# Performance work log

Measured on AMD Instinct MI355X. Metric: run time of the kernel, lower is better.

Reference implementation:

```python
import jax, jax.numpy as jnp
from jax import lax
import numpy as np

A = 9                 # 3 scales x 3 ratios
PRE_NMS_TOPN = 4000
POST_NMS_TOPN = 2000
NMS_THRESH = 0.7
MIN_SIZE = 16.0       # min_size * im_scale (im_info scale = 1)
NEG_INF = -1e9


def generate_anchors(base_size=16, ratios=(0.5, 1.0, 2.0), scales=(8, 16, 32)):
    ratios = np.array(ratios, dtype=np.float64)
    scales = np.array(scales, dtype=np.float64)
    w = h = float(base_size)
    xc = yc = 0.5 * (base_size - 1)
    size = w * h
    ws_r = np.round(np.sqrt(size / ratios))          # [3]
    hs_r = np.round(ws_r * ratios)                   # [3]
    ws = (ws_r[:, None] * scales[None, :]).reshape(-1)   # [9]
    hs = (hs_r[:, None] * scales[None, :]).reshape(-1)   # [9]
    anchors = np.stack([xc - 0.5 * (ws - 1), yc - 0.5 * (hs - 1),
                        xc + 0.5 * (ws - 1), yc + 0.5 * (hs - 1)], axis=1)
    return anchors.astype(np.float32)                # [9,4]


def _conv(x, w, b, padding):
    y = lax.conv_general_dilated(x, w, (1, 1), padding,
                                 dimension_numbers=('NCHW', 'OIHW', 'NCHW'))
    return y + b[None, :, None, None]


def _bbox_transform_inv(anchors, deltas):
    w = anchors[:, 2] - anchors[:, 0] + 1.0
    h = anchors[:, 3] - anchors[:, 1] + 1.0
    cx = anchors[:, 0] + 0.5 * w
    cy = anchors[:, 1] + 0.5 * h
    pcx = deltas[:, 0] * w + cx
    pcy = deltas[:, 1] * h + cy
    pw = jnp.exp(deltas[:, 2]) * w
    ph = jnp.exp(deltas[:, 3]) * h
    return jnp.stack([pcx - 0.5 * pw, pcy - 0.5 * ph,
                      pcx + 0.5 * pw, pcy + 0.5 * ph], axis=1)


def _greedy_nms(boxes, keep_init, thresh):
    # boxes already sorted by descending score; keep_init masks invalid rows
    x1, y1, x2, y2 = boxes[:, 0], boxes[:, 1], boxes[:, 2], boxes[:, 3]
    areas = (x2 - x1 + 1.0) * (y2 - y1 + 1.0)
    xx1 = jnp.maximum(x1[:, None], x1[None, :])
    yy1 = jnp.maximum(y1[:, None], y1[None, :])
    xx2 = jnp.minimum(x2[:, None], x2[None, :])
    yy2 = jnp.minimum(y2[:, None], y2[None, :])
    inter = jnp.maximum(0.0, xx2 - xx1 + 1.0) * jnp.maximum(0.0, yy2 - yy1 + 1.0)
    iou = inter / (areas[:, None] + areas[None, :] - inter)   # [N,N]
    n = boxes.shape[0]
    idx = jnp.arange(n)

    def body(i, keep):
        suppress = keep[i] & (iou[i] > thresh) & (idx > i)
        return keep & ~suppress

    return lax.fori_loop(0, n, body, keep_init)


def reference(im, feats, w_conv, b_conv, w_cls, b_cls, w_reg, b_reg):
    im_h, im_w = im.shape[2], im.shape[3]
    fh, fw = feats.shape[2], feats.shape[3]
    stride = round(im_w / fw)

    # RPN head (classifier)
    hid = jax.nn.relu(_conv(feats, w_conv, b_conv, 'SAME'))
    rpn_map = _conv(hid, w_cls, b_cls, 'SAME')       # [1, 2A, fh, fw]
    rpn_bbox = _conv(hid, w_reg, b_reg, 'SAME')      # [1, 4A, fh, fw]

    # anchor generation: [K*A, 4], shift-major / anchor-minor
    base = jnp.asarray(generate_anchors())
    sx = jnp.arange(fw, dtype=jnp.float32) * stride
    sy = jnp.arange(fh, dtype=jnp.float32) * stride
    sxx, syy = jnp.meshgrid(sx, sy)                  # [fh, fw]
    shifts = jnp.stack([sxx.ravel(), syy.ravel(), sxx.ravel(), syy.ravel()], 1)
    anchors = (base[None, :, :] + shifts[:, None, :]).reshape(-1, 4)

    # predictions, flattened in (h, w, a) order to match anchors
    deltas = rpn_bbox.transpose(0, 2, 3, 1).reshape(-1, 4)
    scores = rpn_map[:, A:, :, :].transpose(0, 2, 3, 1).reshape(-1)

    proposals = _bbox_transform_inv(anchors, deltas)
    # clip_boxes to image
    proposals = jnp.stack([
        jnp.clip(proposals[:, 0], 0.0, im_w - 1.0),
        jnp.clip(proposals[:, 1], 0.0, im_h - 1.0),
        jnp.clip(proposals[:, 2], 0.0, im_w - 1.0),
        jnp.clip(proposals[:, 3], 0.0, im_h - 1.0)], axis=1)

    # filter_boxes (min_size) expressed as a score mask (jit-friendly)
    ws = proposals[:, 2] - proposals[:, 0] + 1.0
    hs = proposals[:, 3] - proposals[:, 1] + 1.0
    valid = (ws >= MIN_SIZE) & (hs >= MIN_SIZE)
    masked_scores = jnp.where(valid, scores, NEG_INF)

    # sort descending, take pre_nms_topN
    order = jnp.argsort(-masked_scores)[:PRE_NMS_TOPN]
    top_boxes = proposals[order]
    top_scores = masked_scores[order]
    keep_init = top_scores > NEG_INF / 2

    keep = _greedy_nms(top_boxes, keep_init, NMS_THRESH)

    # take first post_nms_topN kept (already in score order), padded with zeros
    rank = jnp.cumsum(keep) - 1
    take = keep & (rank < POST_NMS_TOPN)
    dst = jnp.where(take, rank, 0)
    out_boxes = jnp.zeros((POST_NMS_TOPN, 4), dtype=top_boxes.dtype)
    out_boxes = out_boxes.at[dst].add(jnp.where(take[:, None], top_boxes, 0.0))
    out_scores = jnp.zeros((POST_NMS_TOPN, 1), dtype=top_scores.dtype)
    out_scores = out_scores.at[dst].add(jnp.where(take[:, None], top_scores[:, None], 0.0))
    return out_boxes, out_scores


def setup_inputs() -> dict:
    key = jax.random.key(0)
    ks = jax.random.split(key, 8)
    # small weight scale keeps exp(dw) in a sane range, as a trained RPN would
    return {
        'im': jax.random.normal(ks[0], (1, 3, 800, 1216), jnp.float32),
        'feats': jax.random.normal(ks[1], (1, 1024, 50, 76), jnp.float32),
        'w_conv': jax.random.normal(ks[2], (512, 1024, 3, 3), jnp.float32) * 0.001,
        'b_conv': jnp.zeros((512,), jnp.float32),
        'w_cls': jax.random.normal(ks[3], (18, 512, 1, 1), jnp.float32) * 0.01,
        'b_cls': jnp.zeros((18,), jnp.float32),
        'w_reg': jax.random.normal(ks[4], (36, 512, 1, 1), jnp.float32) * 0.01,
        'b_reg': jnp.zeros((36,), jnp.float32),
    }
```

## Files before the change

kernel.cpp:

```cpp
#include <hip/hip_runtime.h>
#include <stdint.h>
#include <math.h>

typedef unsigned long long u64;
typedef unsigned int u32;

#define CIN     1024
#define COUT    512
#define FH      50
#define FW      76
#define QP      80
#define HIDP    4096
#define FPITCH  4160
#define NPOS    3800
#define NA      34200
#define PRE_N   4000
#define POST_N  2000
#define MASKW   63
#define TBN     4032
#define KSLICES 8
#define CPS     128
#define QT      128
#define SPP     (CPS/2)

#define P0 (3*CIN*FPITCH)
#define P2 (512*48)
#define P3 65536
#define PREP_BLKS ((P0+P2+P3)/256)
#define WT_BLKS   (144*8)

__device__ __forceinline__ void async16(const float* g, float* l) {
  __builtin_amdgcn_global_load_lds(
      (__attribute__((address_space(1))) void*)(g),
      (__attribute__((address_space(3))) void*)(l), 16, 0, 0);
}

__global__ void k_prep(const float* __restrict__ feats, const float* __restrict__ w_conv,
                       const float* __restrict__ w_cls, const float* __restrict__ b_cls,
                       const float* __restrict__ w_reg, const float* __restrict__ b_reg,
                       float* __restrict__ fpad3, float* __restrict__ wt,
                       float* __restrict__ wT, float* __restrict__ bT,
                       u32* __restrict__ hist, u32* __restrict__ ctrl,
                       double4* __restrict__ tb, float* __restrict__ ts) {
  __shared__ float t[64][65];
  if (blockIdx.x >= PREP_BLKS) {
    int bt_ = blockIdx.x - PREP_BLKS;
    int kx = bt_ % 144, oy = bt_ / 144;
    int k0 = kx * 64, oc0 = oy * 64;
    int tx = threadIdx.x & 63, tg = threadIdx.x >> 6;
#pragma unroll
    for (int rr = 0; rr < 16; rr++) {
      int row = tg * 16 + rr;
      t[row][tx] = w_conv[(size_t)(oc0 + row) * 9216 + k0 + tx];
    }
    __syncthreads();
#pragma unroll
    for (int rr = 0; rr < 16; rr++) {
      int kr = tg * 16 + rr;
      wt[(size_t)(k0 + kr) * 512 + oc0 + tx] = t[tx][kr];
    }
    return;
  }
  int idx = blockIdx.x * 256 + threadIdx.x;
  if (idx < P0) {
    int tc = idx / (CIN * FPITCH);
    int rem = idx - tc * (CIN * FPITCH);
    int cin = rem / FPITCH;
    int j = rem - cin * FPITCH + tc;
    float v = 0.f;
    if (j < FPITCH) {
      int r = j / QP, u = j - r * QP;
      if (r >= 1 && r <= FH && u >= 1 && u <= FW)
        v = feats[cin * (FH * FW) + (r - 1) * FW + (u - 1)];
    }
    fpad3[idx] = v;
    return;
  }
  idx -= P0;
  if (idx < P2) {
    int c = idx / 48, o = idx - c * 48;
    float v = 0.f;
    if (o < 9) v = w_cls[(size_t)(9 + o) * 512 + c];
    else if (o < 45) v = w_reg[(size_t)(o - 9) * 512 + c];
    wT[idx] = v;
    return;
  }
  idx -= P2;
  if (idx < P3) {
    hist[idx] = 0;
    if (idx < 8) ctrl[idx] = 0;
    if (idx < 48) bT[idx] = (idx < 9) ? b_cls[9 + idx] : (idx < 45 ? b_reg[idx - 9] : 0.f);
    if (idx >= PRE_N && idx < TBN) { tb[idx] = make_double4(0.0, 0.0, 0.0, 0.0); ts[idx] = -1.0e9f; }
  }
}

__global__ __launch_bounds__(256, 6) void k_conv(const float* __restrict__ fpad3,
                                                 const float* __restrict__ wt,
                                                 float* __restrict__ hidp) {
  __shared__ __align__(16) float Bl[2][2][10][QT];
  const int tid = threadIdx.x;
  const int lane = tid & 63;
  const int wv = __builtin_amdgcn_readfirstlane(tid >> 6);
  const int q0 = blockIdx.x * QT;
  const int ws = (blockIdx.y << 2) + wv;
  const int c0 = blockIdx.z * CPS;

  int rA = 2 * wv + (lane >> 5);
  int trA = rA / 3, tcA = rA - trA * 3;
  u32 voffA = (u32)tcA * (CIN * FPITCH) + (u32)trA * QP + q0 + (lane & 31) * 4;
  u32 voffB = 2u * (CIN * FPITCH) + 2u * QP + q0 + (lane & 31) * 4;

  float acc32[8][2];
  double acc64[8][2];
#pragma unroll
  for (int i = 0; i < 8; i++) {
    acc32[i][0] = acc32[i][1] = 0.f;
    acc64[i][0] = acc64[i][1] = 0.0;
  }

#define STAGE(buf, sp)  do {                                                    \
    const float* _b0 = fpad3 + (size_t)(c0 + 2 * (sp)) * FPITCH;                \
    async16(_b0 + voffA, &Bl[buf][0][2 * wv][0]);                               \
    if (wv == 0) async16(_b0 + voffB, &Bl[buf][0][8][0]);                       \
    const float* _b1 = _b0 + FPITCH;                                            \
    async16(_b1 + voffA, &Bl[buf][1][2 * wv][0]);                               \
    if (wv == 0) async16(_b1 + voffB, &Bl[buf][1][8][0]);                       \
  } while (0)

  STAGE(0, 0);

#pragma unroll 1
  for (int sp = 0; sp < SPP; sp++) {
    __syncthreads();
    if (sp + 1 < SPP) STAGE((sp + 1) & 1, sp + 1);
    const int b0 = sp & 1;
#pragma unroll
    for (int ci = 0; ci < 2; ci++) {
      const int cin = c0 + 2 * sp + ci;
      const float* wp = wt + (((size_t)cin * 9) << 9) + (ws << 3);
#pragma unroll
      for (int ks = 0; ks < 9; ks++) {
        float2 b2 = *(const float2*)&Bl[b0][ci][ks][lane * 2];
        const float* w8 = wp + (ks << 9);
#pragma unroll
        for (int i = 0; i < 8; i++) {
          float w = w8[i];
          acc32[i][0] = fmaf(w, b2.x, acc32[i][0]);
          acc32[i][1] = fmaf(w, b2.y, acc32[i][1]);
        }
      }
    }
    if ((sp & 3) == 3) {
#pragma unroll
      for (int i = 0; i < 8; i++) {
        acc64[i][0] += (double)acc32[i][0]; acc32[i][0] = 0.f;
        acc64[i][1] += (double)acc32[i][1]; acc32[i][1] = 0.f;
      }
    }
  }
#undef STAGE

#pragma unroll
  for (int i = 0; i < 8; i++) {
    float2 o;
    o.x = (float)acc64[i][0];
    o.y = (float)acc64[i][1];
    *(float2*)&hidp[((size_t)(blockIdx.z * COUT + (ws << 3) + i) << 12) + q0 + lane * 2] = o;
  }
}

__global__ void k_reduce(const float* __restrict__ hidp, const float* __restrict__ bconv,
                         float* __restrict__ hid) {
  int idx = blockIdx.x * 256 + threadIdx.x;
  int oc = idx >> 12;
  double s = 0.0;
#pragma unroll
  for (int z = 0; z < KSLICES; z++)
    s += (double)hidp[idx + ((size_t)z << 21)];
  s += (double)bconv[oc];
  hid[idx] = s > 0.0 ? (float)s : 0.f;
}

__global__ __launch_bounds__(256, 8) void k_head(const float* __restrict__ hid,
                                                 const float* __restrict__ wT,
                                                 const float* __restrict__ bT,
                                                 float* __restrict__ scoresb,
                                                 float* __restrict__ deltab) {
  int lane = threadIdx.x & 63;
  int wv = threadIdx.x >> 6;
  int q = blockIdx.x * 64 + lane;
  int og = blockIdx.y * 12 + wv * 3;
  double acc0 = 0.0, acc1 = 0.0, acc2 = 0.0;
#pragma unroll 4
  for (int c = 0; c < 512; c++) {
    double hv = (double)hid[((size_t)c << 12) + q];
    const float* wr = wT + c * 48 + og;
    acc0 += hv * (double)wr[0];
    acc1 += hv * (double)wr[1];
    acc2 += hv * (double)wr[2];
  }
  int y = q / QP, x = q - y * QP;
  if (x < FW && y < FH) {
    int pos = y * FW + x;
    double a[3] = {acc0, acc1, acc2};
#pragma unroll
    for (int j = 0; j < 3; j++) {
      int o = og + j;
      float r = (float)(a[j] + (double)bT[o]);
      if (o < 9)       scoresb[o * NPOS + pos] = r;
      else if (o < 45) deltab[(o - 9) * NPOS + pos] = r;
    }
  }
}

__device__ __constant__ float AW[9] = {184.f, 368.f, 736.f, 128.f, 256.f, 512.f, 88.f, 176.f, 352.f};
__device__ __constant__ float AH[9] = {96.f, 192.f, 384.f, 128.f, 256.f, 512.f, 176.f, 352.f, 704.f};

__global__ void k_prop(const float* __restrict__ scoresb, const float* __restrict__ deltab,
                       double4* __restrict__ boxesd, u64* __restrict__ keys,
                       float* __restrict__ smask, u32* __restrict__ hist,
                       float* __restrict__ dout) {
  int g = blockIdx.x * 256 + threadIdx.x;
  if (g < 10000) dout[g] = 0.f;
  if (g >= NA) return;
  int pos = g / 9, a = g - pos * 9;
  int y = pos / FW, x = pos - y * FW;
  double w = (double)AW[a], h = (double)AH[a];
  double cx = x * 16.0 + 8.0, cy = y * 16.0 + 8.0;
  double d0 = (double)deltab[(4 * a + 0) * NPOS + pos];
  double d1 = (double)deltab[(4 * a + 1) * NPOS + pos];
  double d2 = (double)deltab[(4 * a + 2) * NPOS + pos];
  double d3 = (double)deltab[(4 * a + 3) * NPOS + pos];
  double pcx = d0 * w + cx, pcy = d1 * h + cy;
  double pw = exp(d2) * w, ph = exp(d3) * h;
  double px1 = fmin(fmax(pcx - 0.5 * pw, 0.0), 1215.0);
  double py1 = fmin(fmax(pcy - 0.5 * ph, 0.0), 799.0);
  double px2 = fmin(fmax(pcx + 0.5 * pw, 0.0), 1215.0);
  double py2 = fmin(fmax(pcy + 0.5 * ph, 0.0), 799.0);
  bool valid = (px2 - px1 + 1.0 >= 16.0) && (py2 - py1 + 1.0 >= 16.0);
  float sc = scoresb[a * NPOS + pos];
  float ms = valid ? sc : -1.0e9f;
  boxesd[g] = make_double4(px1, py1, px2, py2);
  smask[g] = ms;
  u32 u = __float_as_uint(ms);
  u = (u >> 31) ? ~u : (u | 0x80000000u);
  keys[g] = ((u64)u << 32) | (u32)(~(u32)g);
  atomicAdd(&hist[(((u >> 16) & 0xFFu) << 8) | (u >> 24)], 1u);
}

__global__ void k_scan(const u32* __restrict__ hist, u32* __restrict__ ctrl) {
  __shared__ u32 cs[256];
  __shared__ u32 sfx[256];
  int t = threadIdx.x;
  u32 s = 0;
  for (int i = 0; i < 256; i++) s += hist[(i << 8) | t];
  cs[t] = s;
  __syncthreads();
  if (t == 0) {
    u32 c = 0;
    for (int i = 255; i >= 0; i--) { sfx[i] = c; c += cs[i]; }
  }
  __syncthreads();
  u32 before = sfx[t];
  u32 c = 0;
  for (int blo = 255; blo >= 0; blo--) {
    u32 hv = hist[(blo << 8) | t];
    if (before + c < PRE_N && before + c + hv >= PRE_N) {
      ctrl[0] = (u32)(t * 256 + blo);
      ctrl[1] = before + c;
    }
    c += hv;
  }
}

__global__ void k_compact(const u64* __restrict__ keys, u32* __restrict__ ctrl,
                          u64* __restrict__ candK, u32* __restrict__ candG) {
  int g = blockIdx.x * 256 + threadIdx.x;
  if (g >= NA) return;
  u32 binB = ctrl[0];
  u64 k = keys[g];
  if ((u32)(k >> 48) >= binB) {
    u32 idx = atomicAdd(&ctrl[2], 1u);
    candK[idx] = k;
    candG[idx] = g;
  }
}

__global__ void k_rank(const u64* __restrict__ candK, const u32* __restrict__ candG,
                       const u32* __restrict__ ctrl, const double4* __restrict__ boxesd,
                       const float* __restrict__ smask, double4* __restrict__ tb,
                       float* __restrict__ ts) {
  __shared__ u64 kk[256];
  u32 m = ctrl[2];
  if (blockIdx.x * 256 >= m) return;
  int i = blockIdx.x * 256 + threadIdx.x;
  u64 my = (i < (int)m) ? candK[i] : 0ULL;
  u32 rank = 0;
  for (u32 base = 0; base < m; base += 256) {
    u32 j = base + threadIdx.x;
    kk[threadIdx.x] = (j < m) ? candK[j] : 0ULL;
    __syncthreads();
    u32 lim = m - base; if (lim > 256) lim = 256;
    for (u32 tt = 0; tt < lim; tt++) rank += (kk[tt] > my) ? 1u : 0u;
    __syncthreads();
  }
  if (i < (int)m && rank < PRE_N) {
    u32 g = candG[i];
    tb[rank] = boxesd[g];
    ts[rank] = smask[g];
  }
}

__global__ void k_mask(const double4* __restrict__ tb, u64* __restrict__ mask) {
  __shared__ double4 bx[64];
  int w = blockIdx.x;
  int i = blockIdx.y * 256 + threadIdx.x;
  if (threadIdx.x < 64) bx[threadIdx.x] = tb[w * 64 + threadIdx.x];
  __syncthreads();
  if (i >= PRE_N) return;
  double4 b = tb[i];
  double ai = (b.z - b.x + 1.0) * (b.w - b.y + 1.0);
  u64 word = 0;
#pragma unroll 8
  for (int j = 0; j < 64; j++) {
    int jg = w * 64 + j;
    double4 cc = bx[j];
    double xx1 = fmax(b.x, cc.x), yy1 = fmax(b.y, cc.y);
    double xx2 = fmin(b.z, cc.z), yy2 = fmin(b.w, cc.w);
    double iw = xx2 - xx1 + 1.0, ih = yy2 - yy1 + 1.0;
    iw = iw > 0.0 ? iw : 0.0; ih = ih > 0.0 ? ih : 0.0;
    double inter = iw * ih;
    double aj = (cc.z - cc.x + 1.0) * (cc.w - cc.y + 1.0);
    bool sup = (jg > i) && (inter > 0.7 * (ai + aj - inter));
    word |= sup ? (1ULL << j) : 0ULL;
  }
  mask[(size_t)i * MASKW + w] = word;
}

__global__ __launch_bounds__(64, 1) void k_nms(const u64* __restrict__ mask,
                                               const float* __restrict__ ts,
                                               const double4* __restrict__ tb,
                                               float* __restrict__ out) {
  int lane = threadIdx.x;
  u64 keep = 0;
  for (int w = 0; w < MASKW; w++) {
    float s = ts[w * 64 + lane];
    u64 b = __ballot(s > -5.0e8f);
    if (lane == w) keep = b;
  }
  const bool ldok = (lane < MASKW);
#pragma unroll 1
  for (int c = 0; c < MASKW; c++) {
    u64 v[64];
#pragma unroll
    for (int j = 0; j < 64; j++)
      v[j] = ldok ? mask[(size_t)(c * 64 + j) * MASKW + lane] : 0ULL;
    u64 cur = (u64)(u32)__builtin_amdgcn_readlane((int)(u32)keep, c)
            | ((u64)(u32)__builtin_amdgcn_readlane((int)(u32)(keep >> 32), c) << 32);
#pragma unroll
    for (int j = 0; j < 64; j++) {
      u64 Dj = (u64)(u32)__builtin_amdgcn_readlane((int)(u32)v[j], c)
             | ((u64)(u32)__builtin_amdgcn_readlane((int)(u32)(v[j] >> 32), c) << 32);
      u64 msk = (u64)0 - ((cur >> j) & 1ULL);
      cur &= ~(Dj & msk);
    }
    if (lane == c) keep = cur;
    u64 supp = 0;
#pragma unroll
    for (int j = 0; j < 64; j++) {
      u64 msk = (u64)0 - ((cur >> j) & 1ULL);
      supp |= v[j] & msk;
    }
    keep &= ~supp;
  }
  int pc = __popcll(keep);
  int pre = pc;
#pragma unroll
  for (int off = 1; off < 64; off <<= 1) {
    int v2 = __shfl_up(pre, off);
    if (lane >= off) pre += v2;
  }
  pre -= pc;
#pragma unroll 1
  for (int j = 0; j < 64; j++) {
    if ((keep >> j) & 1ULL) {
      int r = pre + __popcll(keep & ((1ULL << j) - 1ULL));
      if (r < POST_N) {
        int i = lane * 64 + j;
        double4 b = tb[i];
        out[r * 4 + 0] = (float)b.x;
        out[r * 4 + 1] = (float)b.y;
        out[r * 4 + 2] = (float)b.z;
        out[r * 4 + 3] = (float)b.w;
        out[8000 + r] = ts[i];
      }
    }
  }
}

extern "C" void kernel_launch(void* const* d_in, const int* in_sizes, int n_in,
                              void* d_out, int out_size, void* d_ws, size_t ws_size,
                              hipStream_t stream) {
  const float* feats  = (const float*)d_in[1];
  const float* w_conv = (const float*)d_in[2];
  const float* b_conv = (const float*)d_in[3];
  const float* w_cls  = (const float*)d_in[4];
  const float* b_cls  = (const float*)d_in[5];
  const float* w_reg  = (const float*)d_in[6];
  const float* b_reg  = (const float*)d_in[7];
  float* out = (float*)d_out;

  char* p = (char*)d_ws;
  auto carve = [&p](size_t bytes) -> void* {
    void* r = (void*)p;
    p += (bytes + 255) & ~(size_t)255;
    return r;
  };
  float*   fpad3   = (float*)carve(sizeof(float) * (P0 + 512));
  float*   wt      = (float*)carve(sizeof(float) * 9216 * 512);
  float*   wT      = (float*)carve(sizeof(float) * P2);
  float*   bT      = (float*)carve(sizeof(float) * 48);
  float*   hid     = (float*)carve(sizeof(float) * COUT * HIDP);
  float*   hidp    = (float*)carve(sizeof(float) * KSLICES * COUT * HIDP);
  float*   scoresb = (float*)carve(sizeof(float) * 9 * NPOS);
  float*   deltab  = (float*)carve(sizeof(float) * 36 * NPOS);
  double4* boxesd  = (double4*)carve(sizeof(double4) * NA);
  u64*     keys    = (u64*)carve(sizeof(u64) * NA);
  float*   smask   = (float*)carve(sizeof(float) * NA);
  u32*     hist    = (u32*)carve(sizeof(u32) * 65536);
  u32*     ctrl    = (u32*)carve(256);
  u64*     candK   = (u64*)carve(sizeof(u64) * NA);
  u32*     candG   = (u32*)carve(sizeof(u32) * NA);
  double4* tb      = (double4*)carve(sizeof(double4) * TBN);
  float*   ts      = (float*)carve(sizeof(float) * TBN);
  u64*     maskb   = (u64*)carve(sizeof(u64) * (size_t)TBN * MASKW);
  (void)ws_size; (void)in_sizes; (void)n_in; (void)out_size;

  k_prep<<<PREP_BLKS + WT_BLKS, 256, 0, stream>>>(feats, w_conv, w_cls, b_cls, w_reg, b_reg,
                                                  fpad3, wt, wT, bT, hist, ctrl, tb, ts);
  k_conv<<<dim3(32, 16, KSLICES), 256, 0, stream>>>(fpad3, wt, hidp);
  k_reduce<<<8192, 256, 0, stream>>>(hidp, b_conv, hid);
  k_head<<<dim3(64, 4), 256, 0, stream>>>(hid, wT, bT, scoresb, deltab);
  k_prop<<<134, 256, 0, stream>>>(scoresb, deltab, boxesd, keys, smask, hist, out);
  k_scan<<<1, 256, 0, stream>>>(hist, ctrl);
  k_compact<<<134, 256, 0, stream>>>(keys, ctrl, candK, candG);
  k_rank<<<134, 256, 0, stream>>>(candK, candG, ctrl, boxesd, smask, tb, ts);
  k_mask<<<dim3(MASKW, 16), 256, 0, stream>>>(tb, maskb);
  k_nms<<<1, 64, 0, stream>>>(maskb, ts, tb, out);
}
```

Measured before the change: 958.2 us.

## Fuse post-processing kernels into one persistent kernel with grid barriers

```diff
diff --git a/kernel.cpp b/kernel.cpp
--- a/kernel.cpp
+++ b/kernel.cpp
@@ -216,183 +216,207 @@
 __device__ __constant__ float AW[9] = {184.f, 368.f, 736.f, 128.f, 256.f, 512.f, 88.f, 176.f, 352.f};
 __device__ __constant__ float AH[9] = {96.f, 192.f, 384.f, 128.f, 256.f, 512.f, 176.f, 352.f, 704.f};
 
-__global__ void k_prop(const float* __restrict__ scoresb, const float* __restrict__ deltab,
-                       double4* __restrict__ boxesd, u64* __restrict__ keys,
-                       float* __restrict__ smask, u32* __restrict__ hist,
-                       float* __restrict__ dout) {
-  int g = blockIdx.x * 256 + threadIdx.x;
-  if (g < 10000) dout[g] = 0.f;
-  if (g >= NA) return;
-  int pos = g / 9, a = g - pos * 9;
-  int y = pos / FW, x = pos - y * FW;
-  double w = (double)AW[a], h = (double)AH[a];
-  double cx = x * 16.0 + 8.0, cy = y * 16.0 + 8.0;
-  double d0 = (double)deltab[(4 * a + 0) * NPOS + pos];
-  double d1 = (double)deltab[(4 * a + 1) * NPOS + pos];
-  double d2 = (double)deltab[(4 * a + 2) * NPOS + pos];
-  double d3 = (double)deltab[(4 * a + 3) * NPOS + pos];
-  double pcx = d0 * w + cx, pcy = d1 * h + cy;
-  double pw = exp(d2) * w, ph = exp(d3) * h;
-  double px1 = fmin(fmax(pcx - 0.5 * pw, 0.0), 1215.0);
-  double py1 = fmin(fmax(pcy - 0.5 * ph, 0.0), 799.0);
-  double px2 = fmin(fmax(pcx + 0.5 * pw, 0.0), 1215.0);
-  double py2 = fmin(fmax(pcy + 0.5 * ph, 0.0), 799.0);
-  bool valid = (px2 - px1 + 1.0 >= 16.0) && (py2 - py1 + 1.0 >= 16.0);
-  float sc = scoresb[a * NPOS + pos];
-  float ms = valid ? sc : -1.0e9f;
-  boxesd[g] = make_double4(px1, py1, px2, py2);
-  smask[g] = ms;
-  u32 u = __float_as_uint(ms);
-  u = (u >> 31) ? ~u : (u | 0x80000000u);
-  keys[g] = ((u64)u << 32) | (u32)(~(u32)g);
-  atomicAdd(&hist[(((u >> 16) & 0xFFu) << 8) | (u >> 24)], 1u);
-}
-
-__global__ void k_scan(const u32* __restrict__ hist, u32* __restrict__ ctrl) {
+__device__ __forceinline__ void gbar(u32* cnt, u32 target) {
+  __syncthreads();
+  if (threadIdx.x == 0) {
+    __threadfence();
+    atomicAdd(cnt, 1u);
+    while (atomicAdd(cnt, 0u) < target) __builtin_amdgcn_s_sleep(2);
+  }
+  __syncthreads();
+  __threadfence();
+}
+
+__global__ __launch_bounds__(256, 2) void k_post(const float* __restrict__ scoresb,
+                                                 const float* __restrict__ deltab,
+                                                 double4* __restrict__ boxesd,
+                                                 u64* __restrict__ keys,
+                                                 float* __restrict__ smask,
+                                                 u32* __restrict__ hist,
+                                                 u32* __restrict__ ctrl,
+                                                 u64* __restrict__ candK,
+                                                 u32* __restrict__ candG,
+                                                 double4* __restrict__ tb,
+                                                 float* __restrict__ ts,
+                                                 u64* __restrict__ maskb,
+                                                 float* __restrict__ out) {
   __shared__ u32 cs[256];
   __shared__ u32 sfx[256];
-  int t = threadIdx.x;
-  u32 s = 0;
-  for (int i = 0; i < 256; i++) s += hist[(i << 8) | t];
-  cs[t] = s;
-  __syncthreads();
-  if (t == 0) {
+  __shared__ u64 kk[256];
+  __shared__ double4 bx[64];
+  u32* bcnt = &ctrl[7];
+  const int tid = threadIdx.x;
+  int g = blockIdx.x * 256 + tid;
+
+  if (g < 10000) out[g] = 0.f;
+  if (g < NA) {
+    int pos = g / 9, a = g - pos * 9;
+    int y = pos / FW, x = pos - y * FW;
+    double w = (double)AW[a], h = (double)AH[a];
+    double cx = x * 16.0 + 8.0, cy = y * 16.0 + 8.0;
+    double d0 = (double)deltab[(4 * a + 0) * NPOS + pos];
+    double d1 = (double)deltab[(4 * a + 1) * NPOS + pos];
+    double d2 = (double)deltab[(4 * a + 2) * NPOS + pos];
+    double d3 = (double)deltab[(4 * a + 3) * NPOS + pos];
+    double pcx = d0 * w + cx, pcy = d1 * h + cy;
+    double pw = exp(d2) * w, ph = exp(d3) * h;
+    double px1 = fmin(fmax(pcx - 0.5 * pw, 0.0), 1215.0);
+    double py1 = fmin(fmax(pcy - 0.5 * ph, 0.0), 799.0);
+    double px2 = fmin(fmax(pcx + 0.5 * pw, 0.0), 1215.0);
+    double py2 = fmin(fmax(pcy + 0.5 * ph, 0.0), 799.0);
+    bool valid = (px2 - px1 + 1.0 >= 16.0) && (py2 - py1 + 1.0 >= 16.0);
+    float sc = scoresb[a * NPOS + pos];
+    float ms = valid ? sc : -1.0e9f;
+    boxesd[g] = make_double4(px1, py1, px2, py2);
+    smask[g] = ms;
+    u32 u = __float_as_uint(ms);
+    u = (u >> 31) ? ~u : (u | 0x80000000u);
+    keys[g] = ((u64)u << 32) | (u32)(~(u32)g);
+    atomicAdd(&hist[(((u >> 16) & 0xFFu) << 8) | (u >> 24)], 1u);
+  }
+  gbar(bcnt, 256);
+
+  if (blockIdx.x == 0) {
+    u32 s = 0;
+    for (int i = 0; i < 256; i++) s += hist[(i << 8) | tid];
+    cs[tid] = s;
+    __syncthreads();
+    if (tid == 0) {
+      u32 c = 0;
+      for (int i = 255; i >= 0; i--) { sfx[i] = c; c += cs[i]; }
+    }
+    __syncthreads();
+    u32 before = sfx[tid];
     u32 c = 0;
-    for (int i = 255; i >= 0; i--) { sfx[i] = c; c += cs[i]; }
-  }
-  __syncthreads();
-  u32 before = sfx[t];
-  u32 c = 0;
-  for (int blo = 255; blo >= 0; blo--) {
-    u32 hv = hist[(blo << 8) | t];
-    if (before + c < PRE_N && before + c + hv >= PRE_N) {
-      ctrl[0] = (u32)(t * 256 + blo);
-      ctrl[1] = before + c;
-    }
-    c += hv;
-  }
-}
-
-__global__ void k_compact(const u64* __restrict__ keys, u32* __restrict__ ctrl,
-                          u64* __restrict__ candK, u32* __restrict__ candG) {
-  int g = blockIdx.x * 256 + threadIdx.x;
-  if (g >= NA) return;
-  u32 binB = ctrl[0];
-  u64 k = keys[g];
-  if ((u32)(k >> 48) >= binB) {
-    u32 idx = atomicAdd(&ctrl[2], 1u);
-    candK[idx] = k;
-    candG[idx] = g;
-  }
-}
-
-__global__ void k_rank(const u64* __restrict__ candK, const u32* __restrict__ candG,
-                       const u32* __restrict__ ctrl, const double4* __restrict__ boxesd,
-                       const float* __restrict__ smask, double4* __restrict__ tb,
-                       float* __restrict__ ts) {
-  __shared__ u64 kk[256];
-  u32 m = ctrl[2];
-  if (blockIdx.x * 256 >= m) return;
-  int i = blockIdx.x * 256 + threadIdx.x;
-  u64 my = (i < (int)m) ? candK[i] : 0ULL;
-  u32 rank = 0;
-  for (u32 base = 0; base < m; base += 256) {
-    u32 j = base + threadIdx.x;
-    kk[threadIdx.x] = (j < m) ? candK[j] : 0ULL;
-    __syncthreads();
-    u32 lim = m - base; if (lim > 256) lim = 256;
-    for (u32 tt = 0; tt < lim; tt++) rank += (kk[tt] > my) ? 1u : 0u;
-    __syncthreads();
-  }
-  if (i < (int)m && rank < PRE_N) {
-    u32 g = candG[i];
-    tb[rank] = boxesd[g];
-    ts[rank] = smask[g];
-  }
-}
-
-__global__ void k_mask(const double4* __restrict__ tb, u64* __restrict__ mask) {
-  __shared__ double4 bx[64];
-  int w = blockIdx.x;
-  int i = blockIdx.y * 256 + threadIdx.x;
-  if (threadIdx.x < 64) bx[threadIdx.x] = tb[w * 64 + threadIdx.x];
-  __syncthreads();
-  if (i >= PRE_N) return;
-  double4 b = tb[i];
-  double ai = (b.z - b.x + 1.0) * (b.w - b.y + 1.0);
-  u64 word = 0;
+    for (int blo = 255; blo >= 0; blo--) {
+      u32 hv = hist[(blo << 8) | tid];
+      if (before + c < PRE_N && before + c + hv >= PRE_N) {
+        ctrl[0] = (u32)(tid * 256 + blo);
+        ctrl[1] = before + c;
+      }
+      c += hv;
+    }
+  }
+  gbar(bcnt, 512);
+
+  if (g < NA) {
+    u32 binB = ctrl[0];
+    u64 k = keys[g];
+    if ((u32)(k >> 48) >= binB) {
+      u32 idx = atomicAdd(&ctrl[2], 1u);
+      candK[idx] = k;
+      candG[idx] = g;
+    }
+  }
+  gbar(bcnt, 768);
+
+  {
+    u32 m = ctrl[2];
+    if (blockIdx.x * 256 < (int)m) {
+      int i = blockIdx.x * 256 + tid;
+      u64 my = (i < (int)m) ? candK[i] : 0ULL;
+      u32 rank = 0;
+      for (u32 base = 0; base < m; base += 256) {
+        u32 j = base + tid;
+        kk[tid] = (j < m) ? candK[j] : 0ULL;
+        __syncthreads();
+        u32 lim = m - base; if (lim > 256) lim = 256;
+        for (u32 tt = 0; tt < lim; tt++) rank += (kk[tt] > my) ? 1u : 0u;
+        __syncthreads();
+      }
+      if (i < (int)m && rank < PRE_N) {
+        u32 gg = candG[i];
+        tb[rank] = boxesd[gg];
+        ts[rank] = smask[gg];
+      }
+    }
+  }
+  gbar(bcnt, 1024);
+
+#pragma unroll 1
+  for (int u0 = blockIdx.x; u0 < MASKW * 16; u0 += 256) {
+    int w = u0 % MASKW, ib = u0 / MASKW;
+    __syncthreads();
+    if (tid < 64) bx[tid] = tb[w * 64 + tid];
+    __syncthreads();
+    int i = ib * 256 + tid;
+    if (i < PRE_N) {
+      double4 b = tb[i];
+      double ai = (b.z - b.x + 1.0) * (b.w - b.y + 1.0);
+      u64 word = 0;
 #pragma unroll 8
-  for (int j = 0; j < 64; j++) {
-    int jg = w * 64 + j;
-    double4 cc = bx[j];
-    double xx1 = fmax(b.x, cc.x), yy1 = fmax(b.y, cc.y);
-    double xx2 = fmin(b.z, cc.z), yy2 = fmin(b.w, cc.w);
-    double iw = xx2 - xx1 + 1.0, ih = yy2 - yy1 + 1.0;
-    iw = iw > 0.0 ? iw : 0.0; ih = ih > 0.0 ? ih : 0.0;
-    double inter = iw * ih;
-    double aj = (cc.z - cc.x + 1.0) * (cc.w - cc.y + 1.0);
-    bool sup = (jg > i) && (inter > 0.7 * (ai + aj - inter));
-    word |= sup ? (1ULL << j) : 0ULL;
-  }
-  mask[(size_t)i * MASKW + w] = word;
-}
-
-__global__ __launch_bounds__(64, 1) void k_nms(const u64* __restrict__ mask,
-                                               const float* __restrict__ ts,
-                                               const double4* __restrict__ tb,
-                                               float* __restrict__ out) {
-  int lane = threadIdx.x;
-  u64 keep = 0;
-  for (int w = 0; w < MASKW; w++) {
-    float s = ts[w * 64 + lane];
-    u64 b = __ballot(s > -5.0e8f);
-    if (lane == w) keep = b;
-  }
-  const bool ldok = (lane < MASKW);
+      for (int j = 0; j < 64; j++) {
+        int jg = w * 64 + j;
+        double4 cc = bx[j];
+        double xx1 = fmax(b.x, cc.x), yy1 = fmax(b.y, cc.y);
+        double xx2 = fmin(b.z, cc.z), yy2 = fmin(b.w, cc.w);
+        double iw = xx2 - xx1 + 1.0, ih = yy2 - yy1 + 1.0;
+        iw = iw > 0.0 ? iw : 0.0; ih = ih > 0.0 ? ih : 0.0;
+        double inter = iw * ih;
+        double aj = (cc.z - cc.x + 1.0) * (cc.w - cc.y + 1.0);
+        bool sup = (jg > i) && (inter > 0.7 * (ai + aj - inter));
+        word |= sup ? (1ULL << j) : 0ULL;
+      }
+      maskb[(size_t)i * MASKW + w] = word;
+    }
+  }
+  gbar(bcnt, 1280);
+  if (blockIdx.x != 0 || tid >= 64) return;
+
+  {
+    int lane = tid;
+    u64 keep = 0;
+    for (int w = 0; w < MASKW; w++) {
+      float s = ts[w * 64 + lane];
+      u64 b = __ballot(s > -5.0e8f);
+      if (lane == w) keep = b;
+    }
+    const bool ldok = (lane < MASKW);
 #pragma unroll 1
-  for (int c = 0; c < MASKW; c++) {
-    u64 v[64];
-#pragma unroll
-    for (int j = 0; j < 64; j++)
-      v[j] = ldok ? mask[(size_t)(c * 64 + j) * MASKW + lane] : 0ULL;
-    u64 cur = (u64)(u32)__builtin_amdgcn_readlane((int)(u32)keep, c)
-            | ((u64)(u32)__builtin_amdgcn_readlane((int)(u32)(keep >> 32), c) << 32);
-#pragma unroll
+    for (int c = 0; c < MASKW; c++) {
+      u64 v[64];
+#pragma unroll
+      for (int j = 0; j < 64; j++)
+        v[j] = ldok ? maskb[(size_t)(c * 64 + j) * MASKW + lane] : 0ULL;
+      u64 cur = (u64)(u32)__builtin_amdgcn_readlane((int)(u32)keep, c)
+              | ((u64)(u32)__builtin_amdgcn_readlane((int)(u32)(keep >> 32), c) << 32);
+#pragma unroll
+      for (int j = 0; j < 64; j++) {
+        u64 Dj = (u64)(u32)__builtin_amdgcn_readlane((int)(u32)v[j], c)
+               | ((u64)(u32)__builtin_amdgcn_readlane((int)(u32)(v[j] >> 32), c) << 32);
+        u64 msk = (u64)0 - ((cur >> j) & 1ULL);
+        cur &= ~(Dj & msk);
+      }
+      if (lane == c) keep = cur;
+      u64 supp = 0;
+#pragma unroll
+      for (int j = 0; j < 64; j++) {
+        u64 msk = (u64)0 - ((cur >> j) & 1ULL);
+        supp |= v[j] & msk;
+      }
+      keep &= ~supp;
+    }
+    int pc = __popcll(keep);
+    int pre = pc;
+#pragma unroll
+    for (int off = 1; off < 64; off <<= 1) {
+      int v2 = __shfl_up(pre, off);
+      if (lane >= off) pre += v2;
+    }
+    pre -= pc;
+#pragma unroll 1
     for (int j = 0; j < 64; j++) {
-      u64 Dj = (u64)(u32)__builtin_amdgcn_readlane((int)(u32)v[j], c)
-             | ((u64)(u32)__builtin_amdgcn_readlane((int)(u32)(v[j] >> 32), c) << 32);
-      u64 msk = (u64)0 - ((cur >> j) & 1ULL);
-      cur &= ~(Dj & msk);
-    }
-    if (lane == c) keep = cur;
-    u64 supp = 0;
-#pragma unroll
-    for (int j = 0; j < 64; j++) {
-      u64 msk = (u64)0 - ((cur >> j) & 1ULL);
-      supp |= v[j] & msk;
-    }
-    keep &= ~supp;
-  }
-  int pc = __popcll(keep);
-  int pre = pc;
-#pragma unroll
-  for (int off = 1; off < 64; off <<= 1) {
-    int v2 = __shfl_up(pre, off);
-    if (lane >= off) pre += v2;
-  }
-  pre -= pc;
-#pragma unroll 1
-  for (int j = 0; j < 64; j++) {
-    if ((keep >> j) & 1ULL) {
-      int r = pre + __popcll(keep & ((1ULL << j) - 1ULL));
-      if (r < POST_N) {
-        int i = lane * 64 + j;
-        double4 b = tb[i];
-        out[r * 4 + 0] = (float)b.x;
-        out[r * 4 + 1] = (float)b.y;
-        out[r * 4 + 2] = (float)b.z;
-        out[r * 4 + 3] = (float)b.w;
-        out[8000 + r] = ts[i];
+      if ((keep >> j) & 1ULL) {
+        int r = pre + __popcll(keep & ((1ULL << j) - 1ULL));
+        if (r < POST_N) {
+          int i = lane * 64 + j;
+          double4 b = tb[i];
+          out[r * 4 + 0] = (float)b.x;
+          out[r * 4 + 1] = (float)b.y;
+          out[r * 4 + 2] = (float)b.z;
+          out[r * 4 + 3] = (float)b.w;
+          out[8000 + r] = ts[i];
+        }
       }
     }
   }
@@ -441,10 +465,6 @@
   k_conv<<<dim3(32, 16, KSLICES), 256, 0, stream>>>(fpad3, wt, hidp);
   k_reduce<<<8192, 256, 0, stream>>>(hidp, b_conv, hid);
   k_head<<<dim3(64, 4), 256, 0, stream>>>(hid, wT, bT, scoresb, deltab);
-  k_prop<<<134, 256, 0, stream>>>(scoresb, deltab, boxesd, keys, smask, hist, out);
-  k_scan<<<1, 256, 0, stream>>>(hist, ctrl);
-  k_compact<<<134, 256, 0, stream>>>(keys, ctrl, candK, candG);
-  k_rank<<<134, 256, 0, stream>>>(candK, candG, ctrl, boxesd, smask, tb, ts);
-  k_mask<<<dim3(MASKW, 16), 256, 0, stream>>>(tb, maskb);
-  k_nms<<<1, 64, 0, stream>>>(maskb, ts, tb, out);
-}
+  k_post<<<256, 256, 0, stream>>>(scoresb, deltab, boxesd, keys, smask, hist, ctrl,
+                                  candK, candG, tb, ts, maskb, out);
+}
```

Measured after the change: 1.104 ms. 15.2% more time.

## Fuse reduce, scan and NMS into producer kernels via last-block atomic counters

Applied to the files above, without the earlier changes.

```diff
diff --git a/kernel.cpp b/kernel.cpp
--- a/kernel.cpp
+++ b/kernel.cpp
@@ -40,7 +40,7 @@
                        const float* __restrict__ w_reg, const float* __restrict__ b_reg,
                        float* __restrict__ fpad3, float* __restrict__ wt,
                        float* __restrict__ wT, float* __restrict__ bT,
-                       u32* __restrict__ hist, u32* __restrict__ ctrl,
+                       u32* __restrict__ hist, u32* __restrict__ ctrl, u32* __restrict__ cnt,
                        double4* __restrict__ tb, float* __restrict__ ts) {
   __shared__ float t[64][65];
   if (blockIdx.x >= PREP_BLKS) {
@@ -88,7 +88,8 @@
   idx -= P2;
   if (idx < P3) {
     hist[idx] = 0;
-    if (idx < 8) ctrl[idx] = 0;
+    if (idx < 16) ctrl[idx] = 0;
+    if (idx < 512) cnt[idx] = 0;
     if (idx < 48) bT[idx] = (idx < 9) ? b_cls[9 + idx] : (idx < 45 ? b_reg[idx - 9] : 0.f);
     if (idx >= PRE_N && idx < TBN) { tb[idx] = make_double4(0.0, 0.0, 0.0, 0.0); ts[idx] = -1.0e9f; }
   }
@@ -96,8 +97,12 @@
 
 __global__ __launch_bounds__(256, 6) void k_conv(const float* __restrict__ fpad3,
                                                  const float* __restrict__ wt,
-                                                 float* __restrict__ hidp) {
+                                                 const float* __restrict__ bconv,
+                                                 float* __restrict__ hidp,
+                                                 float* __restrict__ hid,
+                                                 u32* __restrict__ cnt) {
   __shared__ __align__(16) float Bl[2][2][10][QT];
+  __shared__ bool lastb;
   const int tid = threadIdx.x;
   const int lane = tid & 63;
   const int wv = __builtin_amdgcn_readfirstlane(tid >> 6);
@@ -167,18 +172,25 @@
     o.y = (float)acc64[i][1];
     *(float2*)&hidp[((size_t)(blockIdx.z * COUT + (ws << 3) + i) << 12) + q0 + lane * 2] = o;
   }
-}
-
-__global__ void k_reduce(const float* __restrict__ hidp, const float* __restrict__ bconv,
-                         float* __restrict__ hid) {
-  int idx = blockIdx.x * 256 + threadIdx.x;
-  int oc = idx >> 12;
-  double s = 0.0;
-#pragma unroll
-  for (int z = 0; z < KSLICES; z++)
-    s += (double)hidp[idx + ((size_t)z << 21)];
-  s += (double)bconv[oc];
-  hid[idx] = s > 0.0 ? (float)s : 0.f;
+
+  __threadfence();
+  if (tid == 0)
+    lastb = (atomicAdd(&cnt[blockIdx.y * 32 + blockIdx.x], 1u) == KSLICES - 1);
+  __syncthreads();
+  if (!lastb) return;
+  __threadfence();
+  const int ocb2 = blockIdx.y << 5;
+#pragma unroll 1
+  for (int e = tid; e < 32 * QT; e += 256) {
+    int oc = ocb2 + (e >> 7);
+    size_t base = ((size_t)oc << 12) + q0 + (e & 127);
+    double s = 0.0;
+#pragma unroll
+    for (int z = 0; z < KSLICES; z++)
+      s += (double)hidp[base + ((size_t)z << 21)];
+    s += (double)bconv[oc];
+    hid[base] = s > 0.0 ? (float)s : 0.f;
+  }
 }
 
 __global__ __launch_bounds__(256, 8) void k_head(const float* __restrict__ hid,
@@ -219,54 +231,58 @@
 __global__ void k_prop(const float* __restrict__ scoresb, const float* __restrict__ deltab,
                        double4* __restrict__ boxesd, u64* __restrict__ keys,
                        float* __restrict__ smask, u32* __restrict__ hist,
-                       float* __restrict__ dout) {
-  int g = blockIdx.x * 256 + threadIdx.x;
-  if (g < 10000) dout[g] = 0.f;
-  if (g >= NA) return;
-  int pos = g / 9, a = g - pos * 9;
-  int y = pos / FW, x = pos - y * FW;
-  double w = (double)AW[a], h = (double)AH[a];
-  double cx = x * 16.0 + 8.0, cy = y * 16.0 + 8.0;
-  double d0 = (double)deltab[(4 * a + 0) * NPOS + pos];
-  double d1 = (double)deltab[(4 * a + 1) * NPOS + pos];
-  double d2 = (double)deltab[(4 * a + 2) * NPOS + pos];
-  double d3 = (double)deltab[(4 * a + 3) * NPOS + pos];
-  double pcx = d0 * w + cx, pcy = d1 * h + cy;
-  double pw = exp(d2) * w, ph = exp(d3) * h;
-  double px1 = fmin(fmax(pcx - 0.5 * pw, 0.0), 1215.0);
-  double py1 = fmin(fmax(pcy - 0.5 * ph, 0.0), 799.0);
-  double px2 = fmin(fmax(pcx + 0.5 * pw, 0.0), 1215.0);
-  double py2 = fmin(fmax(pcy + 0.5 * ph, 0.0), 799.0);
-  bool valid = (px2 - px1 + 1.0 >= 16.0) && (py2 - py1 + 1.0 >= 16.0);
-  float sc = scoresb[a * NPOS + pos];
-  float ms = valid ? sc : -1.0e9f;
-  boxesd[g] = make_double4(px1, py1, px2, py2);
-  smask[g] = ms;
-  u32 u = __float_as_uint(ms);
-  u = (u >> 31) ? ~u : (u | 0x80000000u);
-  keys[g] = ((u64)u << 32) | (u32)(~(u32)g);
-  atomicAdd(&hist[(((u >> 16) & 0xFFu) << 8) | (u >> 24)], 1u);
-}
-
-__global__ void k_scan(const u32* __restrict__ hist, u32* __restrict__ ctrl) {
+                       u32* __restrict__ ctrl, float* __restrict__ dout) {
   __shared__ u32 cs[256];
   __shared__ u32 sfx[256];
-  int t = threadIdx.x;
+  __shared__ bool lastb;
+  const int tid = threadIdx.x;
+  int g = blockIdx.x * 256 + tid;
+  if (g < 10000) dout[g] = 0.f;
+  if (g < NA) {
+    int pos = g / 9, a = g - pos * 9;
+    int y = pos / FW, x = pos - y * FW;
+    double w = (double)AW[a], h = (double)AH[a];
+    double cx = x * 16.0 + 8.0, cy = y * 16.0 + 8.0;
+    double d0 = (double)deltab[(4 * a + 0) * NPOS + pos];
+    double d1 = (double)deltab[(4 * a + 1) * NPOS + pos];
+    double d2 = (double)deltab[(4 * a + 2) * NPOS + pos];
+    double d3 = (double)deltab[(4 * a + 3) * NPOS + pos];
+    double pcx = d0 * w + cx, pcy = d1 * h + cy;
+    double pw = exp(d2) * w, ph = exp(d3) * h;
+    double px1 = fmin(fmax(pcx - 0.5 * pw, 0.0), 1215.0);
+    double py1 = fmin(fmax(pcy - 0.5 * ph, 0.0), 799.0);
+    double px2 = fmin(fmax(pcx + 0.5 * pw, 0.0), 1215.0);
+    double py2 = fmin(fmax(pcy + 0.5 * ph, 0.0), 799.0);
+    bool valid = (px2 - px1 + 1.0 >= 16.0) && (py2 - py1 + 1.0 >= 16.0);
+    float sc = scoresb[a * NPOS + pos];
+    float ms = valid ? sc : -1.0e9f;
+    boxesd[g] = make_double4(px1, py1, px2, py2);
+    smask[g] = ms;
+    u32 u = __float_as_uint(ms);
+    u = (u >> 31) ? ~u : (u | 0x80000000u);
+    keys[g] = ((u64)u << 32) | (u32)(~(u32)g);
+    atomicAdd(&hist[(((u >> 16) & 0xFFu) << 8) | (u >> 24)], 1u);
+  }
+  __threadfence();
+  if (tid == 0) lastb = (atomicAdd(&ctrl[8], 1u) == 133u);
+  __syncthreads();
+  if (!lastb) return;
+  __threadfence();
   u32 s = 0;
-  for (int i = 0; i < 256; i++) s += hist[(i << 8) | t];
-  cs[t] = s;
-  __syncthreads();
-  if (t == 0) {
+  for (int i = 0; i < 256; i++) s += hist[(i << 8) | tid];
+  cs[tid] = s;
+  __syncthreads();
+  if (tid == 0) {
     u32 c = 0;
     for (int i = 255; i >= 0; i--) { sfx[i] = c; c += cs[i]; }
   }
   __syncthreads();
-  u32 before = sfx[t];
+  u32 before = sfx[tid];
   u32 c = 0;
   for (int blo = 255; blo >= 0; blo--) {
-    u32 hv = hist[(blo << 8) | t];
+    u32 hv = hist[(blo << 8) | tid];
     if (before + c < PRE_N && before + c + hv >= PRE_N) {
-      ctrl[0] = (u32)(t * 256 + blo);
+      ctrl[0] = (u32)(tid * 256 + blo);
       ctrl[1] = before + c;
     }
     c += hv;
@@ -311,88 +327,95 @@
   }
 }
 
-__global__ void k_mask(const double4* __restrict__ tb, u64* __restrict__ mask) {
+__global__ void k_mask(const double4* __restrict__ tb, const float* __restrict__ ts,
+                       u64* __restrict__ mask, u32* __restrict__ ctrl,
+                       float* __restrict__ out) {
   __shared__ double4 bx[64];
+  __shared__ bool lastb;
+  const int tid = threadIdx.x;
   int w = blockIdx.x;
-  int i = blockIdx.y * 256 + threadIdx.x;
-  if (threadIdx.x < 64) bx[threadIdx.x] = tb[w * 64 + threadIdx.x];
-  __syncthreads();
-  if (i >= PRE_N) return;
-  double4 b = tb[i];
-  double ai = (b.z - b.x + 1.0) * (b.w - b.y + 1.0);
-  u64 word = 0;
+  int i = blockIdx.y * 256 + tid;
+  if (tid < 64) bx[tid] = tb[w * 64 + tid];
+  __syncthreads();
+  if (i < PRE_N) {
+    double4 b = tb[i];
+    double ai = (b.z - b.x + 1.0) * (b.w - b.y + 1.0);
+    u64 word = 0;
 #pragma unroll 8
-  for (int j = 0; j < 64; j++) {
-    int jg = w * 64 + j;
-    double4 cc = bx[j];
-    double xx1 = fmax(b.x, cc.x), yy1 = fmax(b.y, cc.y);
-    double xx2 = fmin(b.z, cc.z), yy2 = fmin(b.w, cc.w);
-    double iw = xx2 - xx1 + 1.0, ih = yy2 - yy1 + 1.0;
-    iw = iw > 0.0 ? iw : 0.0; ih = ih > 0.0 ? ih : 0.0;
-    double inter = iw * ih;
-    double aj = (cc.z - cc.x + 1.0) * (cc.w - cc.y + 1.0);
-    bool sup = (jg > i) && (inter > 0.7 * (ai + aj - inter));
-    word |= sup ? (1ULL << j) : 0ULL;
-  }
-  mask[(size_t)i * MASKW + w] = word;
-}
-
-__global__ __launch_bounds__(64, 1) void k_nms(const u64* __restrict__ mask,
-                                               const float* __restrict__ ts,
-                                               const double4* __restrict__ tb,
-                                               float* __restrict__ out) {
-  int lane = threadIdx.x;
-  u64 keep = 0;
-  for (int w = 0; w < MASKW; w++) {
-    float s = ts[w * 64 + lane];
-    u64 b = __ballot(s > -5.0e8f);
-    if (lane == w) keep = b;
-  }
-  const bool ldok = (lane < MASKW);
+    for (int j = 0; j < 64; j++) {
+      int jg = w * 64 + j;
+      double4 cc = bx[j];
+      double xx1 = fmax(b.x, cc.x), yy1 = fmax(b.y, cc.y);
+      double xx2 = fmin(b.z, cc.z), yy2 = fmin(b.w, cc.w);
+      double iw = xx2 - xx1 + 1.0, ih = yy2 - yy1 + 1.0;
+      iw = iw > 0.0 ? iw : 0.0; ih = ih > 0.0 ? ih : 0.0;
+      double inter = iw * ih;
+      double aj = (cc.z - cc.x + 1.0) * (cc.w - cc.y + 1.0);
+      bool sup = (jg > i) && (inter > 0.7 * (ai + aj - inter));
+      word |= sup ? (1ULL << j) : 0ULL;
+    }
+    mask[(size_t)i * MASKW + w] = word;
+  }
+  __threadfence();
+  if (tid == 0) lastb = (atomicAdd(&ctrl[9], 1u) == (u32)(MASKW * 16 - 1));
+  __syncthreads();
+  if (!lastb) return;
+  __threadfence();
+  if (tid >= 64) return;
+  {
+    int lane = tid;
+    u64 keep = 0;
+    for (int w2 = 0; w2 < MASKW; w2++) {
+      float s = ts[w2 * 64 + lane];
+      u64 b = __ballot(s > -5.0e8f);
+      if (lane == w2) keep = b;
+    }
+    const bool ldok = (lane < MASKW);
 #pragma unroll 1
-  for (int c = 0; c < MASKW; c++) {
-    u64 v[64];
-#pragma unroll
-    for (int j = 0; j < 64; j++)
-      v[j] = ldok ? mask[(size_t)(c * 64 + j) * MASKW + lane] : 0ULL;
-    u64 cur = (u64)(u32)__builtin_amdgcn_readlane((int)(u32)keep, c)
-            | ((u64)(u32)__builtin_amdgcn_readlane((int)(u32)(keep >> 32), c) << 32);
-#pragma unroll
+    for (int c = 0; c < MASKW; c++) {
+      u64 v[64];
+#pragma unroll
+      for (int j = 0; j < 64; j++)
+        v[j] = ldok ? mask[(size_t)(c * 64 + j) * MASKW + lane] : 0ULL;
+      u64 cur = (u64)(u32)__builtin_amdgcn_readlane((int)(u32)keep, c)
+              | ((u64)(u32)__builtin_amdgcn_readlane((int)(u32)(keep >> 32), c) << 32);
+#pragma unroll
+      for (int j = 0; j < 64; j++) {
+        u64 Dj = (u64)(u32)__builtin_amdgcn_readlane((int)(u32)v[j], c)
+               | ((u64)(u32)__builtin_amdgcn_readlane((int)(u32)(v[j] >> 32), c) << 32);
+        u64 msk = (u64)0 - ((cur >> j) & 1ULL);
+        cur &= ~(Dj & msk);
+      }
+      if (lane == c) keep = cur;
+      u64 supp = 0;
+#pragma unroll
+      for (int j = 0; j < 64; j++) {
+        u64 msk = (u64)0 - ((cur >> j) & 1ULL);
+        supp |= v[j] & msk;
+      }
+      keep &= ~supp;
+    }
+    int pc = __popcll(keep);
+    int pre = pc;
+#pragma unroll
+    for (int off = 1; off < 64; off <<= 1) {
+      int v2 = __shfl_up(pre, off);
+      if (lane >= off) pre += v2;
+    }
+    pre -= pc;
+#pragma unroll 1
     for (int j = 0; j < 64; j++) {
-      u64 Dj = (u64)(u32)__builtin_amdgcn_readlane((int)(u32)v[j], c)
-             | ((u64)(u32)__builtin_amdgcn_readlane((int)(u32)(v[j] >> 32), c) << 32);
-      u64 msk = (u64)0 - ((cur >> j) & 1ULL);
-      cur &= ~(Dj & msk);
-    }
-    if (lane == c) keep = cur;
-    u64 supp = 0;
-#pragma unroll
-    for (int j = 0; j < 64; j++) {
-      u64 msk = (u64)0 - ((cur >> j) & 1ULL);
-      supp |= v[j] & msk;
-    }
-    keep &= ~supp;
-  }
-  int pc = __popcll(keep);
-  int pre = pc;
-#pragma unroll
-  for (int off = 1; off < 64; off <<= 1) {
-    int v2 = __shfl_up(pre, off);
-    if (lane >= off) pre += v2;
-  }
-  pre -= pc;
-#pragma unroll 1
-  for (int j = 0; j < 64; j++) {
-    if ((keep >> j) & 1ULL) {
-      int r = pre + __popcll(keep & ((1ULL << j) - 1ULL));
-      if (r < POST_N) {
-        int i = lane * 64 + j;
-        double4 b = tb[i];
-        out[r * 4 + 0] = (float)b.x;
-        out[r * 4 + 1] = (float)b.y;
-        out[r * 4 + 2] = (float)b.z;
-        out[r * 4 + 3] = (float)b.w;
-        out[8000 + r] = ts[i];
+      if ((keep >> j) & 1ULL) {
+        int r = pre + __popcll(keep & ((1ULL << j) - 1ULL));
+        if (r < POST_N) {
+          int i2 = lane * 64 + j;
+          double4 b = tb[i2];
+          out[r * 4 + 0] = (float)b.x;
+          out[r * 4 + 1] = (float)b.y;
+          out[r * 4 + 2] = (float)b.z;
+          out[r * 4 + 3] = (float)b.w;
+          out[8000 + r] = ts[i2];
+        }
       }
     }
   }
@@ -429,6 +452,7 @@
   float*   smask   = (float*)carve(sizeof(float) * NA);
   u32*     hist    = (u32*)carve(sizeof(u32) * 65536);
   u32*     ctrl    = (u32*)carve(256);
+  u32*     cnt     = (u32*)carve(sizeof(u32) * 512);
   u64*     candK   = (u64*)carve(sizeof(u64) * NA);
   u32*     candG   = (u32*)carve(sizeof(u32) * NA);
   double4* tb      = (double4*)carve(sizeof(double4) * TBN);
@@ -437,14 +461,11 @@
   (void)ws_size; (void)in_sizes; (void)n_in; (void)out_size;
 
   k_prep<<<PREP_BLKS + WT_BLKS, 256, 0, stream>>>(feats, w_conv, w_cls, b_cls, w_reg, b_reg,
-                                                  fpad3, wt, wT, bT, hist, ctrl, tb, ts);
-  k_conv<<<dim3(32, 16, KSLICES), 256, 0, stream>>>(fpad3, wt, hidp);
-  k_reduce<<<8192, 256, 0, stream>>>(hidp, b_conv, hid);
+                                                  fpad3, wt, wT, bT, hist, ctrl, cnt, tb, ts);
+  k_conv<<<dim3(32, 16, KSLICES), 256, 0, stream>>>(fpad3, wt, b_conv, hidp, hid, cnt);
   k_head<<<dim3(64, 4), 256, 0, stream>>>(hid, wT, bT, scoresb, deltab);
-  k_prop<<<134, 256, 0, stream>>>(scoresb, deltab, boxesd, keys, smask, hist, out);
-  k_scan<<<1, 256, 0, stream>>>(hist, ctrl);
+  k_prop<<<134, 256, 0, stream>>>(scoresb, deltab, boxesd, keys, smask, hist, ctrl, out);
   k_compact<<<134, 256, 0, stream>>>(keys, ctrl, candK, candG);
   k_rank<<<134, 256, 0, stream>>>(candK, candG, ctrl, boxesd, smask, tb, ts);
-  k_mask<<<dim3(MASKW, 16), 256, 0, stream>>>(tb, maskb);
-  k_nms<<<1, 64, 0, stream>>>(maskb, ts, tb, out);
-}
+  k_mask<<<dim3(MASKW, 16), 256, 0, stream>>>(tb, ts, maskb, ctrl, out);
+}
```

After: 1.743 ms. 1.82x slower.

## Fuse split-K reduction into head and scan into compaction kernel

Applied to the files above, without the earlier changes.

```diff
diff --git a/kernel.cpp b/kernel.cpp
--- a/kernel.cpp
+++ b/kernel.cpp
@@ -169,44 +169,40 @@
   }
 }
 
-__global__ void k_reduce(const float* __restrict__ hidp, const float* __restrict__ bconv,
-                         float* __restrict__ hid) {
-  int idx = blockIdx.x * 256 + threadIdx.x;
-  int oc = idx >> 12;
-  double s = 0.0;
-#pragma unroll
-  for (int z = 0; z < KSLICES; z++)
-    s += (double)hidp[idx + ((size_t)z << 21)];
-  s += (double)bconv[oc];
-  hid[idx] = s > 0.0 ? (float)s : 0.f;
-}
-
-__global__ __launch_bounds__(256, 8) void k_head(const float* __restrict__ hid,
-                                                 const float* __restrict__ wT,
-                                                 const float* __restrict__ bT,
-                                                 float* __restrict__ scoresb,
-                                                 float* __restrict__ deltab) {
+__global__ __launch_bounds__(256, 4) void k_redhead(const float* __restrict__ hidp,
+                                                    const float* __restrict__ bconv,
+                                                    const float* __restrict__ wT,
+                                                    const float* __restrict__ bT,
+                                                    float* __restrict__ scoresb,
+                                                    float* __restrict__ deltab) {
   int lane = threadIdx.x & 63;
   int wv = threadIdx.x >> 6;
   int q = blockIdx.x * 64 + lane;
-  int og = blockIdx.y * 12 + wv * 3;
-  double acc0 = 0.0, acc1 = 0.0, acc2 = 0.0;
-#pragma unroll 4
+  int og = wv * 12;
+  double acc[12];
+#pragma unroll
+  for (int j = 0; j < 12; j++) acc[j] = 0.0;
+#pragma unroll 2
   for (int c = 0; c < 512; c++) {
-    double hv = (double)hid[((size_t)c << 12) + q];
+    size_t base = ((size_t)c << 12) + q;
+    double s = 0.0;
+#pragma unroll
+    for (int z = 0; z < KSLICES; z++)
+      s += (double)hidp[base + ((size_t)z << 21)];
+    s += (double)bconv[c];
+    float hvf = s > 0.0 ? (float)s : 0.f;
+    double hv = (double)hvf;
     const float* wr = wT + c * 48 + og;
-    acc0 += hv * (double)wr[0];
-    acc1 += hv * (double)wr[1];
-    acc2 += hv * (double)wr[2];
+#pragma unroll
+    for (int j = 0; j < 12; j++) acc[j] += hv * (double)wr[j];
   }
   int y = q / QP, x = q - y * QP;
   if (x < FW && y < FH) {
     int pos = y * FW + x;
-    double a[3] = {acc0, acc1, acc2};
-#pragma unroll
-    for (int j = 0; j < 3; j++) {
+#pragma unroll
+    for (int j = 0; j < 12; j++) {
       int o = og + j;
-      float r = (float)(a[j] + (double)bT[o]);
+      float r = (float)(acc[j] + (double)bT[o]);
       if (o < 9)       scoresb[o * NPOS + pos] = r;
       else if (o < 45) deltab[(o - 9) * NPOS + pos] = r;
     }
@@ -248,9 +244,12 @@
   atomicAdd(&hist[(((u >> 16) & 0xFFu) << 8) | (u >> 24)], 1u);
 }
 
-__global__ void k_scan(const u32* __restrict__ hist, u32* __restrict__ ctrl) {
+__global__ void k_compact(const u64* __restrict__ keys, const u32* __restrict__ hist,
+                          u32* __restrict__ ctrl,
+                          u64* __restrict__ candK, u32* __restrict__ candG) {
   __shared__ u32 cs[256];
   __shared__ u32 sfx[256];
+  __shared__ u32 sbinB;
   int t = threadIdx.x;
   u32 s = 0;
   for (int i = 0; i < 256; i++) s += hist[(i << 8) | t];
@@ -265,24 +264,20 @@
   u32 c = 0;
   for (int blo = 255; blo >= 0; blo--) {
     u32 hv = hist[(blo << 8) | t];
-    if (before + c < PRE_N && before + c + hv >= PRE_N) {
-      ctrl[0] = (u32)(t * 256 + blo);
-      ctrl[1] = before + c;
-    }
+    if (before + c < PRE_N && before + c + hv >= PRE_N)
+      sbinB = (u32)(t * 256 + blo);
     c += hv;
   }
-}
-
-__global__ void k_compact(const u64* __restrict__ keys, u32* __restrict__ ctrl,
-                          u64* __restrict__ candK, u32* __restrict__ candG) {
-  int g = blockIdx.x * 256 + threadIdx.x;
-  if (g >= NA) return;
-  u32 binB = ctrl[0];
-  u64 k = keys[g];
-  if ((u32)(k >> 48) >= binB) {
-    u32 idx = atomicAdd(&ctrl[2], 1u);
-    candK[idx] = k;
-    candG[idx] = g;
+  __syncthreads();
+  u32 binB = sbinB;
+  int g = blockIdx.x * 256 + t;
+  if (g < NA) {
+    u64 k = keys[g];
+    if ((u32)(k >> 48) >= binB) {
+      u32 idx = atomicAdd(&ctrl[2], 1u);
+      candK[idx] = k;
+      candG[idx] = g;
+    }
   }
 }
 
@@ -420,7 +415,6 @@
   float*   wt      = (float*)carve(sizeof(float) * 9216 * 512);
   float*   wT      = (float*)carve(sizeof(float) * P2);
   float*   bT      = (float*)carve(sizeof(float) * 48);
-  float*   hid     = (float*)carve(sizeof(float) * COUT * HIDP);
   float*   hidp    = (float*)carve(sizeof(float) * KSLICES * COUT * HIDP);
   float*   scoresb = (float*)carve(sizeof(float) * 9 * NPOS);
   float*   deltab  = (float*)carve(sizeof(float) * 36 * NPOS);
@@ -439,11 +433,9 @@
   k_prep<<<PREP_BLKS + WT_BLKS, 256, 0, stream>>>(feats, w_conv, w_cls, b_cls, w_reg, b_reg,
                                                   fpad3, wt, wT, bT, hist, ctrl, tb, ts);
   k_conv<<<dim3(32, 16, KSLICES), 256, 0, stream>>>(fpad3, wt, hidp);
-  k_reduce<<<8192, 256, 0, stream>>>(hidp, b_conv, hid);
-  k_head<<<dim3(64, 4), 256, 0, stream>>>(hid, wT, bT, scoresb, deltab);
+  k_redhead<<<64, 256, 0, stream>>>(hidp, b_conv, wT, bT, scoresb, deltab);
   k_prop<<<134, 256, 0, stream>>>(scoresb, deltab, boxesd, keys, smask, hist, out);
-  k_scan<<<1, 256, 0, stream>>>(hist, ctrl);
-  k_compact<<<134, 256, 0, stream>>>(keys, ctrl, candK, candG);
+  k_compact<<<134, 256, 0, stream>>>(keys, hist, ctrl, candK, candG);
   k_rank<<<134, 256, 0, stream>>>(candK, candG, ctrl, boxesd, smask, tb, ts);
   k_mask<<<dim3(MASKW, 16), 256, 0, stream>>>(tb, maskb);
   k_nms<<<1, 64, 0, stream>>>(maskb, ts, tb, out);
```

Measured after the change: 1.075 ms. 12.2% more time.
